# Optimization experiments

Hardware: AMD Instinct MI355X
Metric: run time of the kernel (lower is better)

Reference implementation:

```python
import jax, jax.numpy as jnp
import numpy as np

N = 100000
E = 3200000
NEG_SLOPE = 0.2  # PyG GATConv default


def gat_layer(x, src, dst, W, a_src, a_dst, b, heads, out_ch, concat):
    # per-node linear transform, split into heads: [N, H, C]
    h = (x @ W).reshape(N, heads, out_ch)
    # per-node attention logits: [N, H]
    al_src = jnp.sum(h * a_src, axis=-1)
    al_dst = jnp.sum(h * a_dst, axis=-1)
    # per-edge attention coefficient (x_j = source, x_i = target): [E, H]
    e = jax.nn.leaky_relu(al_src[src] + al_dst[dst], NEG_SLOPE)
    # segment softmax over incoming edges of each destination node
    m = jax.ops.segment_max(e, dst, num_segments=N)
    e = jnp.exp(e - m[dst])
    denom = jax.ops.segment_sum(e, dst, num_segments=N)
    alpha = e / (denom[dst] + 1e-16)
    # weighted message aggregation: scatter-add over dst
    msg = h[src] * alpha[..., None]  # [E, H, C]
    out = jax.ops.segment_sum(msg, dst, num_segments=N)  # [N, H, C]
    out = out.reshape(N, heads * out_ch) if concat else out.mean(axis=1)
    return out + b


def setup_inputs() -> dict:
    key = jax.random.key(0)
    ks = jax.random.split(key, 11)
    return {
        "x": jax.random.normal(ks[0], (N, 2), dtype=jnp.float32),
        "edge_index": jax.random.randint(ks[1], (2, E), 0, N, dtype=jnp.int64),
        "edge_attr": jax.random.normal(ks[2], (E, 1), dtype=jnp.float32),
        "W1": jax.random.normal(ks[3], (2, 32), dtype=jnp.float32) * 0.5,
        "att_src1": jax.random.normal(ks[4], (4, 8), dtype=jnp.float32) * 0.3,
        "att_dst1": jax.random.normal(ks[5], (4, 8), dtype=jnp.float32) * 0.3,
        "b1": jnp.zeros((32,), dtype=jnp.float32),
        "W2": jax.random.normal(ks[6], (32, 2), dtype=jnp.float32) * 0.2,
        "att_src2": jax.random.normal(ks[7], (1, 2), dtype=jnp.float32) * 0.3,
        "att_dst2": jax.random.normal(ks[8], (1, 2), dtype=jnp.float32) * 0.3,
        "b2": jnp.zeros((2,), dtype=jnp.float32),
    }


def reference(x, edge_index, edge_attr, W1, att_src1, att_dst1, b1, W2, att_src2, att_dst2, b2):
    # add self-loops (PyG GATConv default add_self_loops=True)
    loops = jnp.arange(N, dtype=edge_index.dtype)
    src = jnp.concatenate([edge_index[0], loops])
    dst = jnp.concatenate([edge_index[1], loops])
    h = gat_layer(x, src, dst, W1, att_src1, att_dst1, b1, heads=4, out_ch=8, concat=True)
    h = jax.nn.elu(h)
    out = gat_layer(h, src, dst, W2, att_src2, att_dst2, b2, heads=1, out_ch=2, concat=False)
    return out
```

## Files before the change

kernel.cpp:

```cpp
#include <hip/hip_runtime.h>
#include <hip/hip_bf16.h>
#include <math.h>

#define NEG_SLOPE 0.2f
#define BK_BITS 9
#define BK (1 << BK_BITS)
#define SBITS 17
#define SMASK ((1 << SBITS) - 1)
#define CAP 20480
#define RSTRIDE (CAP + 4 * BK)
#define PPT 17

__device__ __forceinline__ float lrelu(float x) { return x > 0.f ? x : NEG_SLOPE * x; }

__global__ void init_bcur(int* __restrict__ bcur, int NB) {
    int i = threadIdx.x;
    if (i < NB) bcur[i] = i * CAP;
}

__global__ __launch_bounds__(256) void bucket_scatter(const int* __restrict__ src,
                                                      const int* __restrict__ dst,
                                                      int* __restrict__ bcur,
                                                      int* __restrict__ pairs, int E) {
    __shared__ int cnt[256], sc[256], off[256], cur[256], gbase[256];
    __shared__ int lpair[4096];
    __shared__ unsigned char lbkt[4096];
    int t = threadIdx.x;
    cnt[t] = 0;
    __syncthreads();

    int E4 = E >> 2;
    const int4* src4 = (const int4*)src;
    const int4* dst4 = (const int4*)dst;
    int base4 = blockIdx.x * 1024;
    int4 d4[4], s4[4];
    bool val[4];
#pragma unroll
    for (int k = 0; k < 4; k++) {
        int i4 = base4 + k * 256 + t;
        val[k] = (i4 < E4);
        if (val[k]) {
            d4[k] = dst4[i4];
            s4[k] = src4[i4];
            atomicAdd(&cnt[d4[k].x >> BK_BITS], 1);
            atomicAdd(&cnt[d4[k].y >> BK_BITS], 1);
            atomicAdd(&cnt[d4[k].z >> BK_BITS], 1);
            atomicAdd(&cnt[d4[k].w >> BK_BITS], 1);
        }
    }
    int dt = -1, st = 0;
    if (blockIdx.x == gridDim.x - 1) {
        int e = (E4 << 2) + t;
        if (e < E) { dt = dst[e]; st = src[e]; atomicAdd(&cnt[dt >> BK_BITS], 1); }
    }
    __syncthreads();

    sc[t] = cnt[t];
    __syncthreads();
    for (int o = 1; o < 256; o <<= 1) {
        int u = (t >= o) ? sc[t - o] : 0;
        __syncthreads();
        sc[t] += u;
        __syncthreads();
    }
    int excl = (t == 0) ? 0 : sc[t - 1];
    off[t] = excl;
    cur[t] = excl;
    if (cnt[t] > 0) gbase[t] = atomicAdd(&bcur[t], cnt[t]);
    __syncthreads();
    int total = sc[255];

#pragma unroll
    for (int k = 0; k < 4; k++) {
        if (val[k]) {
            int b, slot;
            b = d4[k].x >> BK_BITS; slot = atomicAdd(&cur[b], 1);
            lpair[slot] = ((d4[k].x & (BK - 1)) << SBITS) | s4[k].x; lbkt[slot] = (unsigned char)b;
            b = d4[k].y >> BK_BITS; slot = atomicAdd(&cur[b], 1);
            lpair[slot] = ((d4[k].y & (BK - 1)) << SBITS) | s4[k].y; lbkt[slot] = (unsigned char)b;
            b = d4[k].z >> BK_BITS; slot = atomicAdd(&cur[b], 1);
            lpair[slot] = ((d4[k].z & (BK - 1)) << SBITS) | s4[k].z; lbkt[slot] = (unsigned char)b;
            b = d4[k].w >> BK_BITS; slot = atomicAdd(&cur[b], 1);
            lpair[slot] = ((d4[k].w & (BK - 1)) << SBITS) | s4[k].w; lbkt[slot] = (unsigned char)b;
        }
    }
    if (dt >= 0) {
        int b = dt >> BK_BITS;
        int slot = atomicAdd(&cur[b], 1);
        lpair[slot] = ((dt & (BK - 1)) << SBITS) | st; lbkt[slot] = (unsigned char)b;
    }
    __syncthreads();

    for (int i = t; i < total; i += 256) {
        int b = lbkt[i];
        pairs[gbase[b] + (i - off[b])] = lpair[i];
    }
}

__global__ __launch_bounds__(1024) void csr_build(const int* __restrict__ pairs,
                                                  const int* __restrict__ bcur,
                                                  int* __restrict__ row_deg,
                                                  int* __restrict__ csr_src, int N) {
    int b = blockIdx.x;
    int t = threadIdx.x;
    int lo = b * CAP, hi = bcur[b];
    int dbase = b << BK_BITS;
    int ndst = min(BK, N - dbase);
    int base2 = b * RSTRIDE;
    __shared__ int cnt[BK];
    __shared__ int sc[256];
    __shared__ int cur[BK];
    if (t < BK) cnt[t] = 0;
    __syncthreads();

    int myp[PPT];
#pragma unroll
    for (int k = 0; k < PPT; k++) {
        int i = lo + t + k * 1024;
        int p = (i < hi) ? pairs[i] : -1;
        myp[k] = p;
        if (p >= 0) atomicAdd(&cnt[p >> SBITS], 1);
    }
    for (int i = lo + t + PPT * 1024; i < hi; i += 1024)
        atomicAdd(&cnt[pairs[i] >> SBITS], 1);
    __syncthreads();

    int d0 = 0, d1 = 0, a0 = 0, a1 = 0;
    if (t < 256) {
        int i0 = 2 * t, i1 = 2 * t + 1;
        d0 = (i0 < ndst) ? cnt[i0] + 1 : 0;
        d1 = (i1 < ndst) ? cnt[i1] + 1 : 0;
        a0 = (d0 + 3) & ~3;
        a1 = (d1 + 3) & ~3;
        sc[t] = a0 + a1;
    }
    __syncthreads();
    for (int o = 1; o < 256; o <<= 1) {
        int u = 0;
        if (t < 256 && t >= o) u = sc[t - o];
        __syncthreads();
        if (t < 256) sc[t] += u;
        __syncthreads();
    }
    if (t < 256) {
        int excl = (t == 0) ? 0 : sc[t - 1];
        int i0 = 2 * t, i1 = 2 * t + 1;
        if (i0 < ndst) {
            row_deg[dbase + i0] = (excl << 16) | d0;
            csr_src[base2 + excl] = dbase + i0;
            for (int k = d0; k < a0; k++) csr_src[base2 + excl + k] = dbase + i0;
            cur[i0] = excl + 1;
        }
        excl += a0;
        if (i1 < ndst) {
            row_deg[dbase + i1] = (excl << 16) | d1;
            csr_src[base2 + excl] = dbase + i1;
            for (int k = d1; k < a1; k++) csr_src[base2 + excl + k] = dbase + i1;
            cur[i1] = excl + 1;
        }
    }
    __syncthreads();

#pragma unroll
    for (int k = 0; k < PPT; k++) {
        int p = myp[k];
        if (p >= 0) {
            int pos = atomicAdd(&cur[p >> SBITS], 1);
            csr_src[base2 + pos] = p & SMASK;
        }
    }
    for (int i = lo + t + PPT * 1024; i < hi; i += 1024) {
        int p = pairs[i];
        int pos = atomicAdd(&cur[p >> SBITS], 1);
        csr_src[base2 + pos] = p & SMASK;
    }
}

__global__ __launch_bounds__(256) void agg1_dstlane(
        const int* __restrict__ row_deg, const int* __restrict__ csr_src,
        const float2* __restrict__ x2,
        const float* __restrict__ W1, const float* __restrict__ asrc,
        const float* __restrict__ adst, const float* __restrict__ b1,
        const float* __restrict__ W2, const float* __restrict__ as2,
        const float* __restrict__ ad2,
        float2* __restrict__ h2, float* __restrict__ al2d, int N) {
    __shared__ float sW[64], sB[32], sW2[64], sP[4], sQ[4], sPd[4], sQd[4], sA2[4];
    int t = threadIdx.x;
    if (t < 64) { sW[t] = W1[t]; sW2[t] = W2[t]; }
    if (t < 32) sB[t] = b1[t];
    if (t < 2) { sA2[t] = as2[t]; sA2[2 + t] = ad2[t]; }
    if (t < 4) {
        float P = 0.f, Q = 0.f, Pd = 0.f, Qd = 0.f;
#pragma unroll
        for (int k = 0; k < 8; k++) {
            int c = t * 8 + k;
            float a = asrc[c], ad_ = adst[c];
            float w0 = W1[c], w1 = W1[32 + c];
            P += w0 * a; Q += w1 * a;
            Pd += w0 * ad_; Qd += w1 * ad_;
        }
        sP[t] = P; sQ[t] = Q; sPd[t] = Pd; sQd[t] = Qd;
    }
    __syncthreads();

    int tid = blockIdx.x * blockDim.x + t;
    int n = tid >> 2;
    int q = tid & 3;
    if (n >= N) return;
    int rd = row_deg[n];
    int row = (n >> BK_BITS) * RSTRIDE + (rd >> 16);
    int deg = rd & 0xFFFF;

    float2 xd = x2[n];
    float P[4], Q[4], ald[4];
#pragma unroll
    for (int h = 0; h < 4; h++) {
        P[h] = sP[h]; Q[h] = sQ[h];
        ald[h] = xd.x * sPd[h] + xd.y * sQd[h];
    }

    float Sw[4] = {0.f, 0.f, 0.f, 0.f};
    float S0[4] = {0.f, 0.f, 0.f, 0.f};
    float S1[4] = {0.f, 0.f, 0.f, 0.f};
    for (int j = q * 4; j < deg; j += 16) {
        int4 s4 = *(const int4*)(csr_src + row + j);
        float2 xs[4];
        xs[0] = x2[s4.x]; xs[1] = x2[s4.y]; xs[2] = x2[s4.z]; xs[3] = x2[s4.w];
#pragma unroll
        for (int k = 0; k < 4; k++) {
            bool live = (j + k < deg);
#pragma unroll
            for (int h = 0; h < 4; h++) {
                float e = lrelu(fmaf(xs[k].x, P[h], fmaf(xs[k].y, Q[h], ald[h])));
                float w = __expf(fminf(e, 80.f));
                w = live ? w : 0.f;
                Sw[h] += w;
                S0[h] += w * xs[k].x;
                S1[h] += w * xs[k].y;
            }
        }
    }
#pragma unroll
    for (int o = 1; o <= 2; o <<= 1) {
#pragma unroll
        for (int h = 0; h < 4; h++) {
            Sw[h] += __shfl_xor(Sw[h], o);
            S0[h] += __shfl_xor(S0[h], o);
            S1[h] += __shfl_xor(S1[h], o);
        }
    }
    if (q != 0) return;

    float r[4];
#pragma unroll
    for (int h = 0; h < 4; h++) r[h] = 1.f / (Sw[h] + 1e-16f);
    float h20 = 0.f, h21 = 0.f;
#pragma unroll
    for (int c = 0; c < 32; c++) {
        int h = c >> 3;
        float outc = (sW[c] * S0[h] + sW[32 + c] * S1[h]) * r[h];
        float v2 = outc + sB[c];
        v2 = v2 > 0.f ? v2 : __expf(v2) - 1.f;
        h20 = fmaf(v2, sW2[2 * c], h20);
        h21 = fmaf(v2, sW2[2 * c + 1], h21);
    }
    h2[n] = make_float2(h20, h21);
    al2d[n] = h20 * sA2[2] + h21 * sA2[3];
}

__global__ __launch_bounds__(256) void agg2_dstlane(
        const int* __restrict__ row_deg, const int* __restrict__ csr_src,
        const float* __restrict__ al2d, const float2* __restrict__ h2,
        const float* __restrict__ as2, const float* __restrict__ b2,
        float2* __restrict__ out, int N) {
    int tid = blockIdx.x * blockDim.x + threadIdx.x;
    int n = tid >> 2;
    int q = tid & 3;
    if (n >= N) return;
    int rd = row_deg[n];
    int row = (n >> BK_BITS) * RSTRIDE + (rd >> 16);
    int deg = rd & 0xFFFF;
    float ald = al2d[n];
    float a0 = as2[0], a1 = as2[1];

    float wsum = 0.f, ax = 0.f, ay = 0.f;
    for (int j = q * 4; j < deg; j += 16) {
        int4 s4 = *(const int4*)(csr_src + row + j);
        float2 hv[4];
        hv[0] = h2[s4.x]; hv[1] = h2[s4.y]; hv[2] = h2[s4.z]; hv[3] = h2[s4.w];
#pragma unroll
        for (int k = 0; k < 4; k++) {
            float e = lrelu(fmaf(hv[k].x, a0, fmaf(hv[k].y, a1, ald)));
            float w = __expf(fminf(e, 80.f));
            w = (j + k < deg) ? w : 0.f;
            wsum += w;
            ax = fmaf(w, hv[k].x, ax);
            ay = fmaf(w, hv[k].y, ay);
        }
    }
#pragma unroll
    for (int o = 1; o <= 2; o <<= 1) {
        wsum += __shfl_xor(wsum, o);
        ax += __shfl_xor(ax, o);
        ay += __shfl_xor(ay, o);
    }
    if (q != 0) return;
    float inv = 1.f / (wsum + 1e-16f);
    out[n] = make_float2(ax * inv + b2[0], ay * inv + b2[1]);
}

extern "C" void kernel_launch(void* const* d_in, const int* in_sizes, int n_in,
                              void* d_out, int out_size, void* d_ws, size_t ws_size,
                              hipStream_t stream) {
    const float* x     = (const float*)d_in[0];
    const int*   eidx  = (const int*)d_in[1];
    const float* W1    = (const float*)d_in[3];
    const float* asrc1 = (const float*)d_in[4];
    const float* adst1 = (const float*)d_in[5];
    const float* b1    = (const float*)d_in[6];
    const float* W2    = (const float*)d_in[7];
    const float* asrc2 = (const float*)d_in[8];
    const float* adst2 = (const float*)d_in[9];
    const float* b2    = (const float*)d_in[10];

    const int N = in_sizes[0] / 2;
    const int E = in_sizes[1] / 2;
    const int* src = eidx;
    const int* dst = eidx + E;
    const int NB = (N + BK - 1) >> BK_BITS;

    float* w = (float*)d_ws;
    float2* h2    = (float2*)w;
    float*  al2d  = w + 2 * (size_t)N;
    int* ip       = (int*)(w + 3 * (size_t)N);
    int* row_deg  = ip;
    int* bcur     = ip + (size_t)N;
    int* pairs    = ip + (size_t)N + NB;
    int* csr_src  = pairs + (size_t)NB * CAP;

    const int B = 256;
    int E4 = E >> 2;
    int gS = (E4 + 1023) / 1024;
    int gL4 = (4 * N + B - 1) / B;

    init_bcur<<<1, B, 0, stream>>>(bcur, NB);
    bucket_scatter<<<gS, B, 0, stream>>>(src, dst, bcur, pairs, E);
    csr_build<<<NB, 1024, 0, stream>>>(pairs, bcur, row_deg, csr_src, N);

    agg1_dstlane<<<gL4, B, 0, stream>>>(row_deg, csr_src, (const float2*)x,
                                        W1, asrc1, adst1, b1, W2, asrc2, adst2,
                                        h2, al2d, N);
    agg2_dstlane<<<gL4, B, 0, stream>>>(row_deg, csr_src, al2d, h2, asrc2, b2,
                                        (float2*)d_out, N);
}
```

Baseline: 184.8 us.

## Split CSR build into half-bucket blocks and shrink scatter tiles

```diff
diff --git a/kernel.cpp b/kernel.cpp
--- a/kernel.cpp
+++ b/kernel.cpp
@@ -8,8 +8,8 @@
 #define SBITS 17
 #define SMASK ((1 << SBITS) - 1)
 #define CAP 20480
-#define RSTRIDE (CAP + 4 * BK)
-#define PPT 17
+#define HRSTRIDE (CAP + 1024)
+#define EPB 2048
 
 __device__ __forceinline__ float lrelu(float x) { return x > 0.f ? x : NEG_SLOPE * x; }
 
@@ -23,8 +23,8 @@
                                                       int* __restrict__ bcur,
                                                       int* __restrict__ pairs, int E) {
     __shared__ int cnt[256], sc[256], off[256], cur[256], gbase[256];
-    __shared__ int lpair[4096];
-    __shared__ unsigned char lbkt[4096];
+    __shared__ int lpair[EPB];
+    __shared__ unsigned char lbkt[EPB];
     int t = threadIdx.x;
     cnt[t] = 0;
     __syncthreads();
@@ -32,11 +32,11 @@
     int E4 = E >> 2;
     const int4* src4 = (const int4*)src;
     const int4* dst4 = (const int4*)dst;
-    int base4 = blockIdx.x * 1024;
-    int4 d4[4], s4[4];
-    bool val[4];
-#pragma unroll
-    for (int k = 0; k < 4; k++) {
+    int base4 = blockIdx.x * (EPB / 4);
+    int4 d4[2], s4[2];
+    bool val[2];
+#pragma unroll
+    for (int k = 0; k < 2; k++) {
         int i4 = base4 + k * 256 + t;
         val[k] = (i4 < E4);
         if (val[k]) {
@@ -71,7 +71,7 @@
     int total = sc[255];
 
 #pragma unroll
-    for (int k = 0; k < 4; k++) {
+    for (int k = 0; k < 2; k++) {
         if (val[k]) {
             int b, slot;
             b = d4[k].x >> BK_BITS; slot = atomicAdd(&cur[b], 1);
@@ -101,38 +101,29 @@
                                                   const int* __restrict__ bcur,
                                                   int* __restrict__ row_deg,
                                                   int* __restrict__ csr_src, int N) {
-    int b = blockIdx.x;
+    int bh = blockIdx.x;
+    int b = bh >> 1, half = bh & 1;
     int t = threadIdx.x;
     int lo = b * CAP, hi = bcur[b];
-    int dbase = b << BK_BITS;
-    int ndst = min(BK, N - dbase);
-    int base2 = b * RSTRIDE;
-    __shared__ int cnt[BK];
+    int dbase0 = (b << BK_BITS) + (half << 8);
+    int ndst = min(256, N - dbase0);
+    if (ndst <= 0) return;
+    int base2 = bh * HRSTRIDE;
+    __shared__ int cnt[256];
     __shared__ int sc[256];
-    __shared__ int cur[BK];
-    if (t < BK) cnt[t] = 0;
-    __syncthreads();
-
-    int myp[PPT];
-#pragma unroll
-    for (int k = 0; k < PPT; k++) {
-        int i = lo + t + k * 1024;
-        int p = (i < hi) ? pairs[i] : -1;
-        myp[k] = p;
-        if (p >= 0) atomicAdd(&cnt[p >> SBITS], 1);
-    }
-    for (int i = lo + t + PPT * 1024; i < hi; i += 1024)
-        atomicAdd(&cnt[pairs[i] >> SBITS], 1);
-    __syncthreads();
-
-    int d0 = 0, d1 = 0, a0 = 0, a1 = 0;
+    __shared__ int cur[256];
+    if (t < 256) cnt[t] = 0;
+    __syncthreads();
+    for (int i = lo + t; i < hi; i += 1024) {
+        int dl = pairs[i] >> SBITS;
+        if ((dl >> 8) == half) atomicAdd(&cnt[dl & 255], 1);
+    }
+    __syncthreads();
+    int d0 = 0, a0 = 0;
     if (t < 256) {
-        int i0 = 2 * t, i1 = 2 * t + 1;
-        d0 = (i0 < ndst) ? cnt[i0] + 1 : 0;
-        d1 = (i1 < ndst) ? cnt[i1] + 1 : 0;
+        d0 = (t < ndst) ? cnt[t] + 1 : 0;
         a0 = (d0 + 3) & ~3;
-        a1 = (d1 + 3) & ~3;
-        sc[t] = a0 + a1;
+        sc[t] = a0;
     }
     __syncthreads();
     for (int o = 1; o < 256; o <<= 1) {
@@ -142,37 +133,21 @@
         if (t < 256) sc[t] += u;
         __syncthreads();
     }
-    if (t < 256) {
+    if (t < ndst) {
         int excl = (t == 0) ? 0 : sc[t - 1];
-        int i0 = 2 * t, i1 = 2 * t + 1;
-        if (i0 < ndst) {
-            row_deg[dbase + i0] = (excl << 16) | d0;
-            csr_src[base2 + excl] = dbase + i0;
-            for (int k = d0; k < a0; k++) csr_src[base2 + excl + k] = dbase + i0;
-            cur[i0] = excl + 1;
-        }
-        excl += a0;
-        if (i1 < ndst) {
-            row_deg[dbase + i1] = (excl << 16) | d1;
-            csr_src[base2 + excl] = dbase + i1;
-            for (int k = d1; k < a1; k++) csr_src[base2 + excl + k] = dbase + i1;
-            cur[i1] = excl + 1;
-        }
-    }
-    __syncthreads();
-
-#pragma unroll
-    for (int k = 0; k < PPT; k++) {
-        int p = myp[k];
-        if (p >= 0) {
-            int pos = atomicAdd(&cur[p >> SBITS], 1);
+        row_deg[dbase0 + t] = (excl << 16) | d0;
+        csr_src[base2 + excl] = dbase0 + t;
+        for (int k = d0; k < a0; k++) csr_src[base2 + excl + k] = dbase0 + t;
+        cur[t] = excl + 1;
+    }
+    __syncthreads();
+    for (int i = lo + t; i < hi; i += 1024) {
+        int p = pairs[i];
+        int dl = p >> SBITS;
+        if ((dl >> 8) == half) {
+            int pos = atomicAdd(&cur[dl & 255], 1);
             csr_src[base2 + pos] = p & SMASK;
         }
-    }
-    for (int i = lo + t + PPT * 1024; i < hi; i += 1024) {
-        int p = pairs[i];
-        int pos = atomicAdd(&cur[p >> SBITS], 1);
-        csr_src[base2 + pos] = p & SMASK;
     }
 }
 
@@ -208,7 +183,7 @@
     int q = tid & 3;
     if (n >= N) return;
     int rd = row_deg[n];
-    int row = (n >> BK_BITS) * RSTRIDE + (rd >> 16);
+    int row = (n >> 8) * HRSTRIDE + (rd >> 16);
     int deg = rd & 0xFFFF;
 
     float2 xd = x2[n];
@@ -278,7 +253,7 @@
     int q = tid & 3;
     if (n >= N) return;
     int rd = row_deg[n];
-    int row = (n >> BK_BITS) * RSTRIDE + (rd >> 16);
+    int row = (n >> 8) * HRSTRIDE + (rd >> 16);
     int deg = rd & 0xFFFF;
     float ald = al2d[n];
     float a0 = as2[0], a1 = as2[1];
@@ -328,6 +303,7 @@
     const int* src = eidx;
     const int* dst = eidx + E;
     const int NB = (N + BK - 1) >> BK_BITS;
+    const int NH = 2 * NB;
 
     float* w = (float*)d_ws;
     float2* h2    = (float2*)w;
@@ -335,17 +311,17 @@
     int* ip       = (int*)(w + 3 * (size_t)N);
     int* row_deg  = ip;
     int* bcur     = ip + (size_t)N;
-    int* pairs    = ip + (size_t)N + NB;
+    int* pairs    = ip + (size_t)N + 200;
     int* csr_src  = pairs + (size_t)NB * CAP;
 
     const int B = 256;
     int E4 = E >> 2;
-    int gS = (E4 + 1023) / 1024;
+    int gS = (E4 + (EPB / 4) - 1) / (EPB / 4);
     int gL4 = (4 * N + B - 1) / B;
 
     init_bcur<<<1, B, 0, stream>>>(bcur, NB);
     bucket_scatter<<<gS, B, 0, stream>>>(src, dst, bcur, pairs, E);
-    csr_build<<<NB, 1024, 0, stream>>>(pairs, bcur, row_deg, csr_src, N);
+    csr_build<<<NH, 1024, 0, stream>>>(pairs, bcur, row_deg, csr_src, N);
 
     agg1_dstlane<<<gL4, B, 0, stream>>>(row_deg, csr_src, (const float2*)x,
                                         W1, asrc1, adst1, b1, W2, asrc2, adst2,
```

Result: slower. 201.3 us (+8.9%).
